# Performance work log

Measured on AMD Instinct MI355X. Metric: run time of the kernel, lower is better.

The kernel has to match this reference:

```python
import jax, jax.numpy as jnp
import numpy as np
import math

B, LQ, LK, D, H = 4, 2048, 2048, 1024, 16
DH = D // H
SCALE = 1.0 / math.sqrt(DH)          # 1/sqrt(d_head), attn_temp=1.0
SOFTMAX_TEMP = 0.5                    # hardcoded logits/0.5 in source
TOPK_FRAC = 0.1
WSCALE = 0.02


def setup_inputs() -> dict:
    key = jax.random.key(0)
    ks = jax.random.split(key, 8)
    inp = {
        "q_in": jax.random.normal(ks[0], (B, LQ, D), jnp.float32),
        "k_in": jax.random.normal(ks[1], (B, LK, D), jnp.float32),
        # torch.nn.Linear convention: y = x @ W.T + b, W is [out, in]
        "Wq": jax.random.normal(ks[2], (D, D), jnp.float32) * WSCALE,
        "bq": jnp.zeros((D,), jnp.float32),
        "Wk": jax.random.normal(ks[3], (D, D), jnp.float32) * WSCALE,
        "bk": jnp.zeros((D,), jnp.float32),
        "Wv": jax.random.normal(ks[4], (D, D), jnp.float32) * WSCALE,
        "bv": jnp.zeros((D,), jnp.float32),
        "Wo": jax.random.normal(ks[5], (D, D), jnp.float32) * WSCALE,
        "bo": jnp.zeros((D,), jnp.float32),
        "kv_pad_mask": jax.random.randint(ks[6], (B, LK), 0, 10) == 0,
    }
    return inp


def _split_heads(x):
    # [B, L, D] -> [B, H, L, DH]
    Bx, L, _ = x.shape
    return x.reshape(Bx, L, H, DH).transpose(0, 2, 1, 3)


def reference(q_in, k_in, Wq, bq, Wk, bk, Wv, bv, Wo, bo, kv_pad_mask):
    q = _split_heads(q_in @ Wq.T + bq)                # [B,H,Lq,DH]
    k = _split_heads(k_in @ Wk.T + bk)                # [B,H,Lk,DH]
    v = _split_heads(jnp.tanh(k_in @ Wv.T + bv))      # v_in defaults to k_in

    logits = jnp.einsum('bhqd,bhkd->bhqk', q, k) * SCALE
    logits = jnp.where(kv_pad_mask[:, None, None, :], jnp.float32(-10000.0), logits)

    attn = jax.nn.softmax(logits / SOFTMAX_TEMP, axis=-1)

    # top-k mask along kv axis: keep entries >= k-th largest value per row
    kk = max(1, int(math.ceil(LK * TOPK_FRAC)))
    thresh = jax.lax.top_k(attn, kk)[0][..., -1:]     # [B,H,Lq,1]
    attn = attn * (attn >= thresh).astype(attn.dtype)

    # pair_ctx = attn[...,None] * v[:,:,None] ; ctx = pair_ctx.sum(-2)
    # == batched matmul (same math, without materializing the 5-D tensor)
    ctx = jnp.einsum('bhqk,bhkd->bhqd', attn, v) * q  # elementwise gate by q

    out = ctx.transpose(0, 2, 1, 3).reshape(B, LQ, D) @ Wo.T + bo
    return out
```

## Files before the change

kernel.cpp:

```cpp
#include <hip/hip_runtime.h>
#include <math.h>

#define NB   4
#define NH   16
#define DHD  64
#define SL   2048
#define DM   1024
#define TOPK 205

#define S_PER_BH 4194304


typedef unsigned short u16;
typedef short    bf16x8  __attribute__((ext_vector_type(8)));
typedef float    f32x4   __attribute__((ext_vector_type(4)));
typedef u16      ushort8 __attribute__((ext_vector_type(8)));
typedef u16      ushort4v __attribute__((ext_vector_type(4)));

__device__ inline void split2(float x, u16& h, u16& l)
{
    unsigned u = __float_as_uint(x);
    unsigned r = u + 0x7FFF + ((u >> 16) & 1);
    u16 hs = (u16)(r >> 16);
    float hf = __uint_as_float((unsigned)hs << 16);
    float lf = x - hf;
    unsigned ul = __float_as_uint(lf);
    unsigned rl = ul + 0x7FFF + ((ul >> 16) & 1);
    h = hs;
    l = (u16)(rl >> 16);
}

__global__ __launch_bounds__(256) void gemm_proj_mfma(const float* __restrict__ X,
                                                      const float* __restrict__ W,
                                                      const float* __restrict__ bias,
                                                      float* __restrict__ outF,
                                                      u16* __restrict__ outH,
                                                      u16* __restrict__ outL,
                                                      int mode)
{
    __shared__ u16 Ah[128 * 40];
    __shared__ u16 Al[128 * 40];
    __shared__ u16 Bh[128 * 40];
    __shared__ u16 Bl[128 * 40];

    const int t    = threadIdx.x;
    const int lane = t & 63;
    const int wv   = t >> 6;
    const int wm   = (wv & 1) * 64;
    const int wn   = (wv >> 1) * 64;
    const int n0   = blockIdx.x * 128;
    const int m0   = blockIdx.y * 128;
    const int ra   = t >> 1;
    const int ca   = (t & 1) * 16;

    const float* Xp = X + (size_t)(m0 + ra) * DM + ca;
    const float* Wp = W + (size_t)(n0 + ra) * DM + ca;

    f32x4 acc[4][4] = {};

    const int lm   = lane & 15;
    const int koff = (lane >> 4) * 8;

    for (int kb = 0; kb < DM; kb += 32) {
        float4 xv[4], wvv[4];
        #pragma unroll
        for (int q = 0; q < 4; ++q) {
            xv[q]  = *(const float4*)(Xp + kb + q * 4);
            wvv[q] = *(const float4*)(Wp + kb + q * 4);
        }
        __syncthreads();
        ushort8 xh[2], xl[2], wh[2], wl[2];
        #pragma unroll
        for (int g = 0; g < 2; ++g)
            #pragma unroll
            for (int e = 0; e < 8; ++e) {
                u16 h_, l_;
                split2(((const float*)xv)[g * 8 + e], h_, l_);
                xh[g][e] = h_; xl[g][e] = l_;
                split2(((const float*)wvv)[g * 8 + e], h_, l_);
                wh[g][e] = h_; wl[g][e] = l_;
            }
        *(ushort8*)&Ah[ra * 40 + ca]     = xh[0];
        *(ushort8*)&Ah[ra * 40 + ca + 8] = xh[1];
        *(ushort8*)&Al[ra * 40 + ca]     = xl[0];
        *(ushort8*)&Al[ra * 40 + ca + 8] = xl[1];
        *(ushort8*)&Bh[ra * 40 + ca]     = wh[0];
        *(ushort8*)&Bh[ra * 40 + ca + 8] = wh[1];
        *(ushort8*)&Bl[ra * 40 + ca]     = wl[0];
        *(ushort8*)&Bl[ra * 40 + ca + 8] = wl[1];
        __syncthreads();
        bf16x8 a_h[4], a_l[4], b_h[4], b_l[4];
        #pragma unroll
        for (int i = 0; i < 4; ++i) {
            int idx = (wm + i * 16 + lm) * 40 + koff;
            a_h[i] = *(const bf16x8*)&Ah[idx];
            a_l[i] = *(const bf16x8*)&Al[idx];
        }
        #pragma unroll
        for (int j = 0; j < 4; ++j) {
            int jdx = (wn + j * 16 + lm) * 40 + koff;
            b_h[j] = *(const bf16x8*)&Bh[jdx];
            b_l[j] = *(const bf16x8*)&Bl[jdx];
        }
        #pragma unroll
        for (int i = 0; i < 4; ++i)
            #pragma unroll
            for (int j = 0; j < 4; ++j) {
                acc[i][j] = __builtin_amdgcn_mfma_f32_16x16x32_bf16(
                    a_h[i], b_h[j], acc[i][j], 0, 0, 0);
                acc[i][j] = __builtin_amdgcn_mfma_f32_16x16x32_bf16(
                    a_h[i], b_l[j], acc[i][j], 0, 0, 0);
                acc[i][j] = __builtin_amdgcn_mfma_f32_16x16x32_bf16(
                    a_l[i], b_h[j], acc[i][j], 0, 0, 0);
            }
    }

    const int rq = (lane >> 4) * 4;
    #pragma unroll
    for (int j = 0; j < 4; ++j) {
        int n = n0 + wn + j * 16 + lm;
        float bb = bias[n];
        #pragma unroll
        for (int i = 0; i < 4; ++i) {
            #pragma unroll
            for (int r = 0; r < 4; ++r) {
                int m = m0 + wm + i * 16 + rq + r;
                float v = acc[i][j][r] + bb;
                if (mode == 2) {
                    outF[(size_t)m * DM + n] = v;
                } else {
                    if (mode == 1) v = tanhf(v);
                    u16 h_, l_;
                    split2(v, h_, l_);
                    size_t idx = (((size_t)((m >> 11) * NH + (n >> 6))) * SL
                                  + (m & 2047)) * DHD + (n & 63);
                    outH[idx] = h_;
                    outL[idx] = l_;
                }
            }
        }
    }
}

__global__ __launch_bounds__(256) void vtrans(const u16* __restrict__ VH,
                                              const u16* __restrict__ VL,
                                              u16* __restrict__ VTH,
                                              u16* __restrict__ VTL)
{
    __shared__ u16 TH[64 * 72];
    __shared__ u16 TL[64 * 72];
    const int t  = threadIdx.x;
    const int k0 = blockIdx.x * 64;
    const int bh = blockIdx.y;
    const int r  = t >> 2;
    const int c  = (t & 3) * 16;
    size_t ib = ((size_t)bh * SL + k0 + r) * DHD + c;
    *(ushort8*)&TH[r * 72 + c]     = *(const ushort8*)&VH[ib];
    *(ushort8*)&TH[r * 72 + c + 8] = *(const ushort8*)&VH[ib + 8];
    *(ushort8*)&TL[r * 72 + c]     = *(const ushort8*)&VL[ib];
    *(ushort8*)&TL[r * 72 + c + 8] = *(const ushort8*)&VL[ib + 8];
    __syncthreads();
    const int d  = t >> 2;
    const int kc = (t & 3) * 16;
    ushort8 oh[2], ol[2];
    #pragma unroll
    for (int g = 0; g < 2; ++g)
        #pragma unroll
        for (int e = 0; e < 8; ++e) {
            oh[g][e] = TH[(kc + g * 8 + e) * 72 + d];
            ol[g][e] = TL[(kc + g * 8 + e) * 72 + d];
        }
    size_t ob = ((size_t)bh * DHD + d) * SL + k0 + kc;
    *(ushort8*)&VTH[ob]     = oh[0];
    *(ushort8*)&VTH[ob + 8] = oh[1];
    *(ushort8*)&VTL[ob]     = ol[0];
    *(ushort8*)&VTL[ob + 8] = ol[1];
}

__global__ __launch_bounds__(256) void scores_mfma(const u16* __restrict__ QH,
                                                   const u16* __restrict__ QL,
                                                   const u16* __restrict__ KH,
                                                   const u16* __restrict__ KL,
                                                   const int* __restrict__ mask,
                                                   float* __restrict__ S,
                                                   int bh0)
{
    __shared__ u16 Qhs[128 * 40];
    __shared__ u16 Qls[128 * 40];
    __shared__ u16 Khs[128 * 40];
    __shared__ u16 Kls[128 * 40];

    const int t    = threadIdx.x;
    const int lane = t & 63;
    const int wv   = t >> 6;
    const int wm   = (wv & 1) * 64;
    const int wn   = (wv >> 1) * 64;
    const int k0   = blockIdx.x * 128;
    const int q0   = blockIdx.y * 128;
    const int bhid = bh0 + blockIdx.z;

    const int row = t >> 1;
    const int col = (t & 1) * 16;
    const size_t qg = ((size_t)bhid * SL + q0 + row) * DHD + col;
    const size_t kg = ((size_t)bhid * SL + k0 + row) * DHD + col;

    f32x4 acc[4][4] = {};
    const int lm = lane & 15;
    const int ko = (lane >> 4) * 8;

    #pragma unroll
    for (int s = 0; s < 2; ++s) {
        ushort8 qh0 = *(const ushort8*)&QH[qg + s * 32];
        ushort8 qh1 = *(const ushort8*)&QH[qg + s * 32 + 8];
        ushort8 ql0 = *(const ushort8*)&QL[qg + s * 32];
        ushort8 ql1 = *(const ushort8*)&QL[qg + s * 32 + 8];
        ushort8 kh0 = *(const ushort8*)&KH[kg + s * 32];
        ushort8 kh1 = *(const ushort8*)&KH[kg + s * 32 + 8];
        ushort8 kl0 = *(const ushort8*)&KL[kg + s * 32];
        ushort8 kl1 = *(const ushort8*)&KL[kg + s * 32 + 8];
        __syncthreads();
        *(ushort8*)&Qhs[row * 40 + col]     = qh0;
        *(ushort8*)&Qhs[row * 40 + col + 8] = qh1;
        *(ushort8*)&Qls[row * 40 + col]     = ql0;
        *(ushort8*)&Qls[row * 40 + col + 8] = ql1;
        *(ushort8*)&Khs[row * 40 + col]     = kh0;
        *(ushort8*)&Khs[row * 40 + col + 8] = kh1;
        *(ushort8*)&Kls[row * 40 + col]     = kl0;
        *(ushort8*)&Kls[row * 40 + col + 8] = kl1;
        __syncthreads();
        bf16x8 ah[4], al[4], bh_[4], bl_[4];
        #pragma unroll
        for (int i = 0; i < 4; ++i) {
            int idx = (wm + i * 16 + lm) * 40 + ko;
            ah[i] = *(const bf16x8*)&Qhs[idx];
            al[i] = *(const bf16x8*)&Qls[idx];
        }
        #pragma unroll
        for (int j = 0; j < 4; ++j) {
            int jdx = (wn + j * 16 + lm) * 40 + ko;
            bh_[j] = *(const bf16x8*)&Khs[jdx];
            bl_[j] = *(const bf16x8*)&Kls[jdx];
        }
        #pragma unroll
        for (int i = 0; i < 4; ++i)
            #pragma unroll
            for (int j = 0; j < 4; ++j) {
                acc[i][j] = __builtin_amdgcn_mfma_f32_16x16x32_bf16(
                    ah[i], bh_[j], acc[i][j], 0, 0, 0);
                acc[i][j] = __builtin_amdgcn_mfma_f32_16x16x32_bf16(
                    ah[i], bl_[j], acc[i][j], 0, 0, 0);
                acc[i][j] = __builtin_amdgcn_mfma_f32_16x16x32_bf16(
                    al[i], bh_[j], acc[i][j], 0, 0, 0);
            }
    }

    const int rq = (lane >> 4) * 4;
    const int b  = bhid >> 4;
    const size_t zbase = (size_t)blockIdx.z * SL;
    #pragma unroll
    for (int j = 0; j < 4; ++j) {
        int k = k0 + wn + j * 16 + lm;
        int mk = mask[(size_t)b * SL + k];
        #pragma unroll
        for (int i = 0; i < 4; ++i) {
            #pragma unroll
            for (int r = 0; r < 4; ++r) {
                int q = q0 + wm + i * 16 + rq + r;
                float val = mk ? -20000.0f : acc[i][j][r] * 0.25f;
                S[(zbase + q) * SL + k] = val;
            }
        }
    }
}

__global__ __launch_bounds__(256) void softmax_topk(float* __restrict__ S)
{
    const int wave = threadIdx.x >> 6;
    const int lane = threadIdx.x & 63;
    const size_t row = (size_t)blockIdx.x * 4 + wave;
    float4* Sr = (float4*)(S + row * SL);

    float4 v[8];
    #pragma unroll
    for (int i = 0; i < 8; ++i) v[i] = Sr[lane + 64 * i];

    float m = -1e30f;
    #pragma unroll
    for (int i = 0; i < 8; ++i)
        m = fmaxf(m, fmaxf(fmaxf(v[i].x, v[i].y), fmaxf(v[i].z, v[i].w)));
    #pragma unroll
    for (int o = 32; o > 0; o >>= 1) m = fmaxf(m, __shfl_xor(m, o, 64));

    float sum = 0.0f;
    #pragma unroll
    for (int i = 0; i < 8; ++i) {
        v[i].x = __expf(v[i].x - m); v[i].y = __expf(v[i].y - m);
        v[i].z = __expf(v[i].z - m); v[i].w = __expf(v[i].w - m);
        sum += (v[i].x + v[i].y) + (v[i].z + v[i].w);
    }
    #pragma unroll
    for (int o = 32; o > 0; o >>= 1) sum += __shfl_xor(sum, o, 64);
    float inv = 1.0f / sum;
    #pragma unroll
    for (int i = 0; i < 8; ++i) {
        v[i].x *= inv; v[i].y *= inv; v[i].z *= inv; v[i].w *= inv;
    }

    unsigned lo = 0u, hi = __float_as_uint(inv);
    while (lo < hi) {
        unsigned mid = (lo + hi + 1u) >> 1;
        int cnt = 0;
        #pragma unroll
        for (int i = 0; i < 8; ++i) {
            cnt += (__float_as_uint(v[i].x) >= mid);
            cnt += (__float_as_uint(v[i].y) >= mid);
            cnt += (__float_as_uint(v[i].z) >= mid);
            cnt += (__float_as_uint(v[i].w) >= mid);
        }
        #pragma unroll
        for (int o = 32; o > 0; o >>= 1) cnt += __shfl_xor(cnt, o, 64);
        if (cnt >= TOPK) lo = mid; else hi = mid - 1u;
    }

    #pragma unroll
    for (int i = 0; i < 8; ++i) {
        float4 x = v[i];
        x.x = (__float_as_uint(x.x) >= lo) ? x.x : 0.0f;
        x.y = (__float_as_uint(x.y) >= lo) ? x.y : 0.0f;
        x.z = (__float_as_uint(x.z) >= lo) ? x.z : 0.0f;
        x.w = (__float_as_uint(x.w) >= lo) ? x.w : 0.0f;
        u16 h_, l_;
        uint4 pk;
        split2(x.x, h_, l_); pk.x = ((unsigned)h_ << 16) | l_;
        split2(x.y, h_, l_); pk.y = ((unsigned)h_ << 16) | l_;
        split2(x.z, h_, l_); pk.z = ((unsigned)h_ << 16) | l_;
        split2(x.w, h_, l_); pk.w = ((unsigned)h_ << 16) | l_;
        *(uint4*)&Sr[lane + 64 * i] = pk;
    }
}

__global__ __launch_bounds__(256) void av_mfma(const unsigned int* __restrict__ SA,
                                               const u16* __restrict__ VTH,
                                               const u16* __restrict__ VTL,
                                               const u16* __restrict__ QH,
                                               const u16* __restrict__ QL,
                                               float* __restrict__ CTX,
                                               int bh0)
{
    __shared__ u16 Ahs[32 * 72];
    __shared__ u16 Als[32 * 72];
    __shared__ u16 Bhs[64 * 72];
    __shared__ u16 Bls[64 * 72];

    const int t    = threadIdx.x;
    const int lane = t & 63;
    const int wv   = t >> 6;
    const int wm   = (wv & 1) * 16;
    const int wn   = (wv >> 1) * 32;
    const int q0   = blockIdx.x * 32;
    const int z    = blockIdx.y;
    const int bhid = bh0 + z;
    const int b    = bhid >> 4, hh = bhid & 15;

    const int arow = t >> 3;
    const int acol = (t & 7) * 8;
    const int brow = t >> 2;
    const int bcol = (t & 3) * 16;

    const unsigned int* Sp = SA + ((size_t)z * SL + q0 + arow) * SL + acol;
    const u16* Vhp = VTH + ((size_t)bhid * DHD + brow) * SL + bcol;
    const u16* Vlp = VTL + ((size_t)bhid * DHD + brow) * SL + bcol;

    const int lm = lane & 15;
    const int ko = (lane >> 4) * 8;

    f32x4 acc[2] = {};

    for (int kb = 0; kb < SL; kb += 64) {
        uint4 ua0 = *(const uint4*)(Sp + kb);
        uint4 ua1 = *(const uint4*)(Sp + kb + 4);
        ushort8 vh0 = *(const ushort8*)(Vhp + kb);
        ushort8 vh1 = *(const ushort8*)(Vhp + kb + 8);
        ushort8 vl0 = *(const ushort8*)(Vlp + kb);
        ushort8 vl1 = *(const ushort8*)(Vlp + kb + 8);
        __syncthreads();
        ushort4v h0 = { (u16)(ua0.x >> 16), (u16)(ua0.y >> 16),
                        (u16)(ua0.z >> 16), (u16)(ua0.w >> 16) };
        ushort4v l0 = { (u16)ua0.x, (u16)ua0.y, (u16)ua0.z, (u16)ua0.w };
        ushort4v h1 = { (u16)(ua1.x >> 16), (u16)(ua1.y >> 16),
                        (u16)(ua1.z >> 16), (u16)(ua1.w >> 16) };
        ushort4v l1 = { (u16)ua1.x, (u16)ua1.y, (u16)ua1.z, (u16)ua1.w };
        *(ushort4v*)&Ahs[arow * 72 + acol]     = h0;
        *(ushort4v*)&Ahs[arow * 72 + acol + 4] = h1;
        *(ushort4v*)&Als[arow * 72 + acol]     = l0;
        *(ushort4v*)&Als[arow * 72 + acol + 4] = l1;
        *(ushort8*)&Bhs[brow * 72 + bcol]      = vh0;
        *(ushort8*)&Bhs[brow * 72 + bcol + 8]  = vh1;
        *(ushort8*)&Bls[brow * 72 + bcol]      = vl0;
        *(ushort8*)&Bls[brow * 72 + bcol + 8]  = vl1;
        __syncthreads();
        #pragma unroll
        for (int s = 0; s < 2; ++s) {
            int ao = (wm + lm) * 72 + s * 32 + ko;
            bf16x8 a_h = *(const bf16x8*)&Ahs[ao];
            bf16x8 a_l = *(const bf16x8*)&Als[ao];
            #pragma unroll
            for (int j = 0; j < 2; ++j) {
                int bo = (wn + j * 16 + lm) * 72 + s * 32 + ko;
                bf16x8 b_h = *(const bf16x8*)&Bhs[bo];
                bf16x8 b_l = *(const bf16x8*)&Bls[bo];
                acc[j] = __builtin_amdgcn_mfma_f32_16x16x32_bf16(
                    a_h, b_h, acc[j], 0, 0, 0);
                acc[j] = __builtin_amdgcn_mfma_f32_16x16x32_bf16(
                    a_h, b_l, acc[j], 0, 0, 0);
                acc[j] = __builtin_amdgcn_mfma_f32_16x16x32_bf16(
                    a_l, b_h, acc[j], 0, 0, 0);
            }
        }
    }

    const int rq = (lane >> 4) * 4;
    #pragma unroll
    for (int j = 0; j < 2; ++j) {
        int d = wn + j * 16 + lm;
        #pragma unroll
        for (int r = 0; r < 4; ++r) {
            int q = q0 + wm + rq + r;
            size_t gi = ((size_t)bhid * SL + q) * DHD + d;
            float gf = __uint_as_float((unsigned)QH[gi] << 16)
                     + __uint_as_float((unsigned)QL[gi] << 16);
            CTX[((size_t)b * SL + q) * DM + hh * DHD + d] = acc[j][r] * gf;
        }
    }
}

extern "C" void kernel_launch(void* const* d_in, const int* in_sizes, int n_in,
                              void* d_out, int out_size, void* d_ws, size_t ws_size,
                              hipStream_t stream)
{
    const float* q_in = (const float*)d_in[0];
    const float* k_in = (const float*)d_in[1];
    const float* Wq   = (const float*)d_in[2];
    const float* bq   = (const float*)d_in[3];
    const float* Wk   = (const float*)d_in[4];
    const float* bk   = (const float*)d_in[5];
    const float* Wv   = (const float*)d_in[6];
    const float* bv   = (const float*)d_in[7];
    const float* Wo   = (const float*)d_in[8];
    const float* bo   = (const float*)d_in[9];
    const int*   mask = (const int*)d_in[10];
    float* out = (float*)d_out;

    char* wsb = (char*)d_ws;
    u16* QHp  = (u16*)(wsb);
    u16* QLp  = (u16*)(wsb + (size_t)16 * 1024 * 1024);
    u16* KHp  = (u16*)(wsb + (size_t)32 * 1024 * 1024);
    u16* KLp  = (u16*)(wsb + (size_t)48 * 1024 * 1024);
    u16* VTHp = (u16*)(wsb + (size_t)64 * 1024 * 1024);
    u16* VTLp = (u16*)(wsb + (size_t)80 * 1024 * 1024);
    float* CTX = (float*)(wsb + (size_t)96 * 1024 * 1024);
    float* S   = (float*)(wsb + (size_t)128 * 1024 * 1024);
    u16* VHt = (u16*)CTX;
    u16* VLt = VHt + (size_t)8388608;

    long s_cap_floats = (long)(ws_size / 4) - 33554432L;
    int chunk = 64;
    while (chunk > 1 && (long)chunk * (long)S_PER_BH > s_cap_floats) chunk >>= 1;

    dim3 blk(256);
    gemm_proj_mfma<<<dim3(8, 64), blk, 0, stream>>>(q_in, Wq, bq, nullptr, QHp, QLp, 0);
    gemm_proj_mfma<<<dim3(8, 64), blk, 0, stream>>>(k_in, Wk, bk, nullptr, KHp, KLp, 0);
    gemm_proj_mfma<<<dim3(8, 64), blk, 0, stream>>>(k_in, Wv, bv, nullptr, VHt, VLt, 1);
    vtrans<<<dim3(32, 64), blk, 0, stream>>>(VHt, VLt, VTHp, VTLp);

    for (int bh0 = 0; bh0 < NB * NH; bh0 += chunk) {
        scores_mfma<<<dim3(16, 16, chunk), blk, 0, stream>>>(QHp, QLp, KHp, KLp, mask, S, bh0);
        softmax_topk<<<dim3(chunk * 512), blk, 0, stream>>>(S);
        av_mfma<<<dim3(64, chunk), blk, 0, stream>>>((const unsigned int*)S,
                                                     VTHp, VTLp, QHp, QLp, CTX, bh0);
    }

    gemm_proj_mfma<<<dim3(8, 64), blk, 0, stream>>>(CTX, Wo, bo, out, nullptr, nullptr, 2);
}
```

Baseline: 1.773 ms.

## Pre-split inputs to bf16 hi/lo, fuse V transpose into GEMM, widen AV blocks

Adds a split_f32 kernel that converts the inputs and weights into bf16 high/low pairs once, so the projection GEMM loads pre-split u16 data instead of splitting fp32 on every tile. The V projection now writes its output directly in transposed layout, which removes the separate vtrans kernel. The attention-times-V kernel runs with 512 threads, giving each wave one 16x16 tile, and writes the context already split into hi/lo for the output GEMM. The cost is extra split kernels and more global traffic for the hi/lo copies, and the transposed V stores are strided and uncoalesced.

```diff
diff --git a/kernel.cpp b/kernel.cpp
--- a/kernel.cpp
+++ b/kernel.cpp
@@ -30,13 +30,35 @@
     l = (u16)(rl >> 16);
 }
 
-__global__ __launch_bounds__(256) void gemm_proj_mfma(const float* __restrict__ X,
-                                                      const float* __restrict__ W,
-                                                      const float* __restrict__ bias,
-                                                      float* __restrict__ outF,
-                                                      u16* __restrict__ outH,
-                                                      u16* __restrict__ outL,
-                                                      int mode)
+__global__ __launch_bounds__(256) void split_f32(const float* __restrict__ in,
+                                                 u16* __restrict__ oh,
+                                                 u16* __restrict__ ol,
+                                                 int n4)
+{
+    const int stride = gridDim.x * 256;
+    for (int i = blockIdx.x * 256 + threadIdx.x; i < n4; i += stride) {
+        float4 v = ((const float4*)in)[i];
+        u16 h0, l0, h1, l1, h2, l2, h3, l3;
+        split2(v.x, h0, l0);
+        split2(v.y, h1, l1);
+        split2(v.z, h2, l2);
+        split2(v.w, h3, l3);
+        ushort4v h = { h0, h1, h2, h3 };
+        ushort4v l = { l0, l1, l2, l3 };
+        *(ushort4v*)&oh[(size_t)i * 4] = h;
+        *(ushort4v*)&ol[(size_t)i * 4] = l;
+    }
+}
+
+__global__ __launch_bounds__(256) void gemm_mfma(const u16* __restrict__ XH,
+                                                 const u16* __restrict__ XL,
+                                                 const u16* __restrict__ WH,
+                                                 const u16* __restrict__ WL,
+                                                 const float* __restrict__ bias,
+                                                 float* __restrict__ outF,
+                                                 u16* __restrict__ outH,
+                                                 u16* __restrict__ outL,
+                                                 int mode)
 {
     __shared__ u16 Ah[128 * 40];
     __shared__ u16 Al[128 * 40];
@@ -53,8 +75,10 @@
     const int ra   = t >> 1;
     const int ca   = (t & 1) * 16;
 
-    const float* Xp = X + (size_t)(m0 + ra) * DM + ca;
-    const float* Wp = W + (size_t)(n0 + ra) * DM + ca;
+    const u16* XHp = XH + (size_t)(m0 + ra) * DM + ca;
+    const u16* XLp = XL + (size_t)(m0 + ra) * DM + ca;
+    const u16* WHp = WH + (size_t)(n0 + ra) * DM + ca;
+    const u16* WLp = WL + (size_t)(n0 + ra) * DM + ca;
 
     f32x4 acc[4][4] = {};
 
@@ -62,32 +86,23 @@
     const int koff = (lane >> 4) * 8;
 
     for (int kb = 0; kb < DM; kb += 32) {
-        float4 xv[4], wvv[4];
-        #pragma unroll
-        for (int q = 0; q < 4; ++q) {
-            xv[q]  = *(const float4*)(Xp + kb + q * 4);
-            wvv[q] = *(const float4*)(Wp + kb + q * 4);
-        }
-        __syncthreads();
-        ushort8 xh[2], xl[2], wh[2], wl[2];
-        #pragma unroll
-        for (int g = 0; g < 2; ++g)
-            #pragma unroll
-            for (int e = 0; e < 8; ++e) {
-                u16 h_, l_;
-                split2(((const float*)xv)[g * 8 + e], h_, l_);
-                xh[g][e] = h_; xl[g][e] = l_;
-                split2(((const float*)wvv)[g * 8 + e], h_, l_);
-                wh[g][e] = h_; wl[g][e] = l_;
-            }
-        *(ushort8*)&Ah[ra * 40 + ca]     = xh[0];
-        *(ushort8*)&Ah[ra * 40 + ca + 8] = xh[1];
-        *(ushort8*)&Al[ra * 40 + ca]     = xl[0];
-        *(ushort8*)&Al[ra * 40 + ca + 8] = xl[1];
-        *(ushort8*)&Bh[ra * 40 + ca]     = wh[0];
-        *(ushort8*)&Bh[ra * 40 + ca + 8] = wh[1];
-        *(ushort8*)&Bl[ra * 40 + ca]     = wl[0];
-        *(ushort8*)&Bl[ra * 40 + ca + 8] = wl[1];
+        ushort8 xh0 = *(const ushort8*)(XHp + kb);
+        ushort8 xh1 = *(const ushort8*)(XHp + kb + 8);
+        ushort8 xl0 = *(const ushort8*)(XLp + kb);
+        ushort8 xl1 = *(const ushort8*)(XLp + kb + 8);
+        ushort8 wh0 = *(const ushort8*)(WHp + kb);
+        ushort8 wh1 = *(const ushort8*)(WHp + kb + 8);
+        ushort8 wl0 = *(const ushort8*)(WLp + kb);
+        ushort8 wl1 = *(const ushort8*)(WLp + kb + 8);
+        __syncthreads();
+        *(ushort8*)&Ah[ra * 40 + ca]     = xh0;
+        *(ushort8*)&Ah[ra * 40 + ca + 8] = xh1;
+        *(ushort8*)&Al[ra * 40 + ca]     = xl0;
+        *(ushort8*)&Al[ra * 40 + ca + 8] = xl1;
+        *(ushort8*)&Bh[ra * 40 + ca]     = wh0;
+        *(ushort8*)&Bh[ra * 40 + ca + 8] = wh1;
+        *(ushort8*)&Bl[ra * 40 + ca]     = wl0;
+        *(ushort8*)&Bl[ra * 40 + ca + 8] = wl1;
         __syncthreads();
         bf16x8 a_h[4], a_l[4], b_h[4], b_l[4];
         #pragma unroll
@@ -129,52 +144,22 @@
                 if (mode == 2) {
                     outF[(size_t)m * DM + n] = v;
                 } else {
-                    if (mode == 1) v = tanhf(v);
+                    int b = m >> 11, l = m & 2047, hh = n >> 6, d = n & 63;
+                    size_t idx;
+                    if (mode == 1) {
+                        v = tanhf(v);
+                        idx = ((size_t)(b * NH + hh) * DHD + d) * SL + l;
+                    } else {
+                        idx = ((size_t)(b * NH + hh) * SL + l) * DHD + d;
+                    }
                     u16 h_, l_;
                     split2(v, h_, l_);
-                    size_t idx = (((size_t)((m >> 11) * NH + (n >> 6))) * SL
-                                  + (m & 2047)) * DHD + (n & 63);
                     outH[idx] = h_;
                     outL[idx] = l_;
                 }
             }
         }
     }
-}
-
-__global__ __launch_bounds__(256) void vtrans(const u16* __restrict__ VH,
-                                              const u16* __restrict__ VL,
-                                              u16* __restrict__ VTH,
-                                              u16* __restrict__ VTL)
-{
-    __shared__ u16 TH[64 * 72];
-    __shared__ u16 TL[64 * 72];
-    const int t  = threadIdx.x;
-    const int k0 = blockIdx.x * 64;
-    const int bh = blockIdx.y;
-    const int r  = t >> 2;
-    const int c  = (t & 3) * 16;
-    size_t ib = ((size_t)bh * SL + k0 + r) * DHD + c;
-    *(ushort8*)&TH[r * 72 + c]     = *(const ushort8*)&VH[ib];
-    *(ushort8*)&TH[r * 72 + c + 8] = *(const ushort8*)&VH[ib + 8];
-    *(ushort8*)&TL[r * 72 + c]     = *(const ushort8*)&VL[ib];
-    *(ushort8*)&TL[r * 72 + c + 8] = *(const ushort8*)&VL[ib + 8];
-    __syncthreads();
-    const int d  = t >> 2;
-    const int kc = (t & 3) * 16;
-    ushort8 oh[2], ol[2];
-    #pragma unroll
-    for (int g = 0; g < 2; ++g)
-        #pragma unroll
-        for (int e = 0; e < 8; ++e) {
-            oh[g][e] = TH[(kc + g * 8 + e) * 72 + d];
-            ol[g][e] = TL[(kc + g * 8 + e) * 72 + d];
-        }
-    size_t ob = ((size_t)bh * DHD + d) * SL + k0 + kc;
-    *(ushort8*)&VTH[ob]     = oh[0];
-    *(ushort8*)&VTH[ob + 8] = oh[1];
-    *(ushort8*)&VTL[ob]     = ol[0];
-    *(ushort8*)&VTL[ob + 8] = ol[1];
 }
 
 __global__ __launch_bounds__(256) void scores_mfma(const u16* __restrict__ QH,
@@ -339,12 +324,13 @@
     }
 }
 
-__global__ __launch_bounds__(256) void av_mfma(const unsigned int* __restrict__ SA,
+__global__ __launch_bounds__(512) void av_mfma(const unsigned int* __restrict__ SA,
                                                const u16* __restrict__ VTH,
                                                const u16* __restrict__ VTL,
                                                const u16* __restrict__ QH,
                                                const u16* __restrict__ QL,
-                                               float* __restrict__ CTX,
+                                               u16* __restrict__ CTXH,
+                                               u16* __restrict__ CTXL,
                                                int bh0)
 {
     __shared__ u16 Ahs[32 * 72];
@@ -356,16 +342,16 @@
     const int lane = t & 63;
     const int wv   = t >> 6;
     const int wm   = (wv & 1) * 16;
-    const int wn   = (wv >> 1) * 32;
+    const int wn   = (wv >> 1) * 16;
     const int q0   = blockIdx.x * 32;
     const int z    = blockIdx.y;
     const int bhid = bh0 + z;
     const int b    = bhid >> 4, hh = bhid & 15;
 
-    const int arow = t >> 3;
-    const int acol = (t & 7) * 8;
-    const int brow = t >> 2;
-    const int bcol = (t & 3) * 16;
+    const int arow = t >> 4;
+    const int acol = (t & 15) * 4;
+    const int brow = t >> 3;
+    const int bcol = (t & 7) * 8;
 
     const unsigned int* Sp = SA + ((size_t)z * SL + q0 + arow) * SL + acol;
     const u16* Vhp = VTH + ((size_t)bhid * DHD + brow) * SL + bcol;
@@ -374,63 +360,49 @@
     const int lm = lane & 15;
     const int ko = (lane >> 4) * 8;
 
-    f32x4 acc[2] = {};
+    f32x4 acc = {};
 
     for (int kb = 0; kb < SL; kb += 64) {
-        uint4 ua0 = *(const uint4*)(Sp + kb);
-        uint4 ua1 = *(const uint4*)(Sp + kb + 4);
-        ushort8 vh0 = *(const ushort8*)(Vhp + kb);
-        ushort8 vh1 = *(const ushort8*)(Vhp + kb + 8);
-        ushort8 vl0 = *(const ushort8*)(Vlp + kb);
-        ushort8 vl1 = *(const ushort8*)(Vlp + kb + 8);
-        __syncthreads();
-        ushort4v h0 = { (u16)(ua0.x >> 16), (u16)(ua0.y >> 16),
-                        (u16)(ua0.z >> 16), (u16)(ua0.w >> 16) };
-        ushort4v l0 = { (u16)ua0.x, (u16)ua0.y, (u16)ua0.z, (u16)ua0.w };
-        ushort4v h1 = { (u16)(ua1.x >> 16), (u16)(ua1.y >> 16),
-                        (u16)(ua1.z >> 16), (u16)(ua1.w >> 16) };
-        ushort4v l1 = { (u16)ua1.x, (u16)ua1.y, (u16)ua1.z, (u16)ua1.w };
-        *(ushort4v*)&Ahs[arow * 72 + acol]     = h0;
-        *(ushort4v*)&Ahs[arow * 72 + acol + 4] = h1;
-        *(ushort4v*)&Als[arow * 72 + acol]     = l0;
-        *(ushort4v*)&Als[arow * 72 + acol + 4] = l1;
-        *(ushort8*)&Bhs[brow * 72 + bcol]      = vh0;
-        *(ushort8*)&Bhs[brow * 72 + bcol + 8]  = vh1;
-        *(ushort8*)&Bls[brow * 72 + bcol]      = vl0;
-        *(ushort8*)&Bls[brow * 72 + bcol + 8]  = vl1;
+        uint4 ua = *(const uint4*)(Sp + kb);
+        ushort8 vh = *(const ushort8*)(Vhp + kb);
+        ushort8 vl = *(const ushort8*)(Vlp + kb);
+        __syncthreads();
+        ushort4v h0 = { (u16)(ua.x >> 16), (u16)(ua.y >> 16),
+                        (u16)(ua.z >> 16), (u16)(ua.w >> 16) };
+        ushort4v l0 = { (u16)ua.x, (u16)ua.y, (u16)ua.z, (u16)ua.w };
+        *(ushort4v*)&Ahs[arow * 72 + acol] = h0;
+        *(ushort4v*)&Als[arow * 72 + acol] = l0;
+        *(ushort8*)&Bhs[brow * 72 + bcol]  = vh;
+        *(ushort8*)&Bls[brow * 72 + bcol]  = vl;
         __syncthreads();
         #pragma unroll
         for (int s = 0; s < 2; ++s) {
             int ao = (wm + lm) * 72 + s * 32 + ko;
             bf16x8 a_h = *(const bf16x8*)&Ahs[ao];
             bf16x8 a_l = *(const bf16x8*)&Als[ao];
-            #pragma unroll
-            for (int j = 0; j < 2; ++j) {
-                int bo = (wn + j * 16 + lm) * 72 + s * 32 + ko;
-                bf16x8 b_h = *(const bf16x8*)&Bhs[bo];
-                bf16x8 b_l = *(const bf16x8*)&Bls[bo];
-                acc[j] = __builtin_amdgcn_mfma_f32_16x16x32_bf16(
-                    a_h, b_h, acc[j], 0, 0, 0);
-                acc[j] = __builtin_amdgcn_mfma_f32_16x16x32_bf16(
-                    a_h, b_l, acc[j], 0, 0, 0);
-                acc[j] = __builtin_amdgcn_mfma_f32_16x16x32_bf16(
-                    a_l, b_h, acc[j], 0, 0, 0);
-            }
+            int bo = (wn + lm) * 72 + s * 32 + ko;
+            bf16x8 b_h = *(const bf16x8*)&Bhs[bo];
+            bf16x8 b_l = *(const bf16x8*)&Bls[bo];
+            acc = __builtin_amdgcn_mfma_f32_16x16x32_bf16(a_h, b_h, acc, 0, 0, 0);
+            acc = __builtin_amdgcn_mfma_f32_16x16x32_bf16(a_h, b_l, acc, 0, 0, 0);
+            acc = __builtin_amdgcn_mfma_f32_16x16x32_bf16(a_l, b_h, acc, 0, 0, 0);
         }
     }
 
     const int rq = (lane >> 4) * 4;
-    #pragma unroll
-    for (int j = 0; j < 2; ++j) {
-        int d = wn + j * 16 + lm;
-        #pragma unroll
-        for (int r = 0; r < 4; ++r) {
-            int q = q0 + wm + rq + r;
-            size_t gi = ((size_t)bhid * SL + q) * DHD + d;
-            float gf = __uint_as_float((unsigned)QH[gi] << 16)
-                     + __uint_as_float((unsigned)QL[gi] << 16);
-            CTX[((size_t)b * SL + q) * DM + hh * DHD + d] = acc[j][r] * gf;
-        }
+    const int d  = wn + lm;
+    #pragma unroll
+    for (int r = 0; r < 4; ++r) {
+        int q = q0 + wm + rq + r;
+        size_t gi = ((size_t)bhid * SL + q) * DHD + d;
+        float gf = __uint_as_float((unsigned)QH[gi] << 16)
+                 + __uint_as_float((unsigned)QL[gi] << 16);
+        float cv = acc[r] * gf;
+        u16 h_, l_;
+        split2(cv, h_, l_);
+        size_t ci = ((size_t)b * SL + q) * DM + hh * DHD + d;
+        CTXH[ci] = h_;
+        CTXL[ci] = l_;
     }
 }
 
@@ -452,33 +424,59 @@
     float* out = (float*)d_out;
 
     char* wsb = (char*)d_ws;
+    const size_t MB = 1024 * 1024;
     u16* QHp  = (u16*)(wsb);
-    u16* QLp  = (u16*)(wsb + (size_t)16 * 1024 * 1024);
-    u16* KHp  = (u16*)(wsb + (size_t)32 * 1024 * 1024);
-    u16* KLp  = (u16*)(wsb + (size_t)48 * 1024 * 1024);
-    u16* VTHp = (u16*)(wsb + (size_t)64 * 1024 * 1024);
-    u16* VTLp = (u16*)(wsb + (size_t)80 * 1024 * 1024);
-    float* CTX = (float*)(wsb + (size_t)96 * 1024 * 1024);
-    float* S   = (float*)(wsb + (size_t)128 * 1024 * 1024);
-    u16* VHt = (u16*)CTX;
-    u16* VLt = VHt + (size_t)8388608;
+    u16* QLp  = (u16*)(wsb + 16 * MB);
+    u16* KHp  = (u16*)(wsb + 32 * MB);
+    u16* KLp  = (u16*)(wsb + 48 * MB);
+    u16* VTHp = (u16*)(wsb + 64 * MB);
+    u16* VTLp = (u16*)(wsb + 80 * MB);
+    u16* CTXH = (u16*)(wsb + 96 * MB);
+    u16* CTXL = (u16*)(wsb + 112 * MB);
+    float* S  = (float*)(wsb + 128 * MB);
+
+    u16* XqH = VTHp;
+    u16* XqL = VTLp;
+    u16* XkH = CTXH;
+    u16* XkL = CTXL;
+    u16* WqH = (u16*)(wsb + 128 * MB);
+    u16* WqL = (u16*)(wsb + 130 * MB);
+    u16* WkH = (u16*)(wsb + 132 * MB);
+    u16* WkL = (u16*)(wsb + 134 * MB);
+    u16* WvH = (u16*)(wsb + 136 * MB);
+    u16* WvL = (u16*)(wsb + 138 * MB);
+    u16* WoH = (u16*)(wsb + 128 * MB);
+    u16* WoL = (u16*)(wsb + 130 * MB);
 
     long s_cap_floats = (long)(ws_size / 4) - 33554432L;
     int chunk = 64;
     while (chunk > 1 && (long)chunk * (long)S_PER_BH > s_cap_floats) chunk >>= 1;
 
     dim3 blk(256);
-    gemm_proj_mfma<<<dim3(8, 64), blk, 0, stream>>>(q_in, Wq, bq, nullptr, QHp, QLp, 0);
-    gemm_proj_mfma<<<dim3(8, 64), blk, 0, stream>>>(k_in, Wk, bk, nullptr, KHp, KLp, 0);
-    gemm_proj_mfma<<<dim3(8, 64), blk, 0, stream>>>(k_in, Wv, bv, nullptr, VHt, VLt, 1);
-    vtrans<<<dim3(32, 64), blk, 0, stream>>>(VHt, VLt, VTHp, VTLp);
+
+    split_f32<<<dim3(2048), blk, 0, stream>>>(q_in, XqH, XqL, 2097152);
+    split_f32<<<dim3(2048), blk, 0, stream>>>(k_in, XkH, XkL, 2097152);
+    split_f32<<<dim3(1024), blk, 0, stream>>>(Wq, WqH, WqL, 262144);
+    split_f32<<<dim3(1024), blk, 0, stream>>>(Wk, WkH, WkL, 262144);
+    split_f32<<<dim3(1024), blk, 0, stream>>>(Wv, WvH, WvL, 262144);
+
+    gemm_mfma<<<dim3(8, 64), blk, 0, stream>>>(XqH, XqL, WqH, WqL, bq,
+                                               nullptr, QHp, QLp, 0);
+    gemm_mfma<<<dim3(8, 64), blk, 0, stream>>>(XkH, XkL, WkH, WkL, bk,
+                                               nullptr, KHp, KLp, 0);
+    gemm_mfma<<<dim3(8, 64), blk, 0, stream>>>(XkH, XkL, WvH, WvL, bv,
+                                               nullptr, VTHp, VTLp, 1);
 
     for (int bh0 = 0; bh0 < NB * NH; bh0 += chunk) {
-        scores_mfma<<<dim3(16, 16, chunk), blk, 0, stream>>>(QHp, QLp, KHp, KLp, mask, S, bh0);
+        scores_mfma<<<dim3(16, 16, chunk), blk, 0, stream>>>(QHp, QLp, KHp, KLp,
+                                                             mask, S, bh0);
         softmax_topk<<<dim3(chunk * 512), blk, 0, stream>>>(S);
-        av_mfma<<<dim3(64, chunk), blk, 0, stream>>>((const unsigned int*)S,
-                                                     VTHp, VTLp, QHp, QLp, CTX, bh0);
-    }
-
-    gemm_proj_mfma<<<dim3(8, 64), blk, 0, stream>>>(CTX, Wo, bo, out, nullptr, nullptr, 2);
-}
+        av_mfma<<<dim3(64, chunk), dim3(512), 0, stream>>>((const unsigned int*)S,
+                                                           VTHp, VTLp, QHp, QLp,
+                                                           CTXH, CTXL, bh0);
+    }
+
+    split_f32<<<dim3(1024), blk, 0, stream>>>(Wo, WoH, WoL, 262144);
+    gemm_mfma<<<dim3(8, 64), blk, 0, stream>>>(CTXH, CTXL, WoH, WoL, bo,
+                                               out, nullptr, nullptr, 2);
+}
```

Result: faster. 1.652 ms (-6.8%).
